# Kernel tuning notes

Measured on AMD Instinct MI355X. Metric: run time of the kernel, lower is better.

## Reference

```python
import jax, jax.numpy as jnp
import numpy as np
import math

B, D_MODEL, SEQ_LEN, EMB_DIM, ORDER = 4, 1024, 4096, 5, 64


def setup_inputs() -> dict:
    key = jax.random.key(0)
    ks = jax.random.split(key, 12)
    L = SEQ_LEN
    # PositionalEmbedding: z = [t, Re(e^{-i f w}), Im(e^{-i f w})]
    t = jnp.linspace(0.0, 1.0, L)[None, :, None]                      # [1,L,1]
    bands = (EMB_DIM - 1) // 2
    t_rescaled = jnp.linspace(0.0, L - 1, L)[None, :, None]           # [1,L,1]
    w = 2 * math.pi * t_rescaled / L
    f = jnp.linspace(1e-4, bands - 1, bands)[None, None]              # [1,1,bands]
    zc = jnp.exp(-1j * f * w.astype(jnp.complex64))                   # [1,L,bands]
    z = jnp.concatenate([t, zc.real, zc.imag], axis=-1)               # [1,L,EMB_DIM]
    # ExponentialModulation deltas (fast_decay_pct=0.3, slow_decay_pct=1.5, target=0.01)
    max_decay = math.log(0.01) / 0.3
    min_decay = math.log(0.01) / 1.5
    deltas = jnp.linspace(min_decay, max_decay, D_MODEL)[None, None]  # [1,1,D]
    s = 0.1  # small init scale for MLP weights
    return {
        "x": jax.random.normal(ks[0], (B, D_MODEL, SEQ_LEN), jnp.float32),
        "L": SEQ_LEN,
        "z": z.astype(jnp.float32),
        "t": t.astype(jnp.float32),
        "deltas": deltas.astype(jnp.float32),
        "W1": jax.random.normal(ks[1], (ORDER, EMB_DIM), jnp.float32) * s,
        "b1": jax.random.normal(ks[2], (ORDER,), jnp.float32) * s,
        "freq": jnp.ones((1, ORDER), jnp.float32),  # Sin freq, w=1
        "W2": jax.random.normal(ks[3], (ORDER, ORDER), jnp.float32) * s,
        "b2": jax.random.normal(ks[4], (ORDER,), jnp.float32) * s,
        "W3": jax.random.normal(ks[5], (ORDER, ORDER), jnp.float32) * s,
        "b3": jax.random.normal(ks[6], (ORDER,), jnp.float32) * s,
        "W4": jax.random.normal(ks[7], (D_MODEL, ORDER), jnp.float32) * s,
        "bias": jax.random.normal(ks[8], (D_MODEL,), jnp.float32),
    }


def reference(x, L, z, t, deltas, W1, b1, freq, W2, b2, W3, b3, W4, bias):
    # --- implicit filter MLP: z [1,L,E] -> k [1,L,D] ---
    zL, tL = z[:, :L], t[:, :L]
    h = jnp.sin(freq * (jnp.einsum('ble,oe->blo', zL, W1) + b1))
    h = jnp.sin(freq * (jnp.einsum('blo,po->blp', h, W2) + b2))
    h = jnp.sin(freq * (jnp.einsum('blo,po->blp', h, W3) + b3))
    h = jnp.einsum('blo,do->bld', h, W4)                # [1,L,D], no bias
    # --- exponential modulation ---
    decay = jnp.exp(-tL * jnp.abs(deltas))              # [1,L,D]
    h = h * decay
    k = h[0].T                                          # [D, L] per-channel filters
    # --- FFT causal conv: irfft(rfft(u)*rfft(k)/n, norm='forward') == plain circular conv on 2L ---
    n = 2 * L
    u_f = jnp.fft.rfft(x, n=n)                          # [B,D,L+1] complex
    k_f = jnp.fft.rfft(k, n=n)                          # [D,L+1]
    y = jnp.fft.irfft(u_f * k_f, n=n)[..., :L]          # [B,D,L]
    out = y + x * bias[:, None]                         # D.unsqueeze(-1) bias term, gelu=False
    return out.astype(x.dtype)
```

## Files before the change

kernel.cpp:

```cpp
#include <hip/hip_runtime.h>
#include <math.h>


#define PAD(i) ((i) + ((i) >> 3))
#define TWO_PI 6.2831853071795864769f

typedef float2 cplx;

__device__ __forceinline__ cplx cmul(cplx a, cplx b) {
    return make_float2(a.x * b.x - a.y * b.y, a.x * b.y + a.y * b.x);
}

__device__ __forceinline__ void dft8(cplx v[8], float sgn) {
    cplx t;
    t = v[1]; v[1] = v[4]; v[4] = t;
    t = v[3]; v[3] = v[6]; v[6] = t;
#pragma unroll
    for (int i = 0; i < 8; i += 2) {
        cplx a = v[i], b = v[i + 1];
        v[i]     = make_float2(a.x + b.x, a.y + b.y);
        v[i + 1] = make_float2(a.x - b.x, a.y - b.y);
    }
#pragma unroll
    for (int i = 0; i < 8; i += 4) {
        cplx a = v[i], b = v[i + 2];
        v[i]     = make_float2(a.x + b.x, a.y + b.y);
        v[i + 2] = make_float2(a.x - b.x, a.y - b.y);
        cplx c1 = v[i + 1], d = v[i + 3];
        cplx dt = make_float2(-sgn * d.y, sgn * d.x);
        v[i + 1] = make_float2(c1.x + dt.x, c1.y + dt.y);
        v[i + 3] = make_float2(c1.x - dt.x, c1.y - dt.y);
    }
    const float C = 0.70710678118654752440f;
    cplx a, b, bt;
    a = v[0]; b = v[4];
    v[0] = make_float2(a.x + b.x, a.y + b.y);
    v[4] = make_float2(a.x - b.x, a.y - b.y);
    a = v[1]; b = v[5]; bt = cmul(b, make_float2(C, sgn * C));
    v[1] = make_float2(a.x + bt.x, a.y + bt.y);
    v[5] = make_float2(a.x - bt.x, a.y - bt.y);
    a = v[2]; b = v[6]; bt = make_float2(-sgn * b.y, sgn * b.x);
    v[2] = make_float2(a.x + bt.x, a.y + bt.y);
    v[6] = make_float2(a.x - bt.x, a.y - bt.y);
    a = v[3]; b = v[7]; bt = cmul(b, make_float2(-C, sgn * C));
    v[3] = make_float2(a.x + bt.x, a.y + bt.y);
    v[7] = make_float2(a.x - bt.x, a.y - bt.y);
}

template <int NS>
__device__ __forceinline__ void fft_pass_ip(cplx* buf, int j, float sgn) {
    cplx v[8];
#pragma unroll
    for (int r = 0; r < 8; r++) v[r] = buf[PAD(j + (r << 9))];
    if (NS > 1) {
        int jm = j & (NS - 1);
        float ang = sgn * (TWO_PI / (float)(NS * 8)) * (float)jm;
#pragma unroll
        for (int r = 1; r < 8; r++) {
            float s, c;
            __sincosf(ang * (float)r, &s, &c);
            v[r] = cmul(v[r], make_float2(c, s));
        }
    }
    dft8(v, sgn);
    __syncthreads();
    int jm2 = j & (NS - 1);
    int base = ((j & ~(NS - 1)) << 3) + jm2;
#pragma unroll
    for (int r = 0; r < 8; r++) buf[PAD(base + r * NS)] = v[r];
    __syncthreads();
}

__device__ __forceinline__ void fft4096_ip(cplx* buf, int t, float sgn) {
    fft_pass_ip<1>(buf, t, sgn);
    fft_pass_ip<8>(buf, t, sgn);
    fft_pass_ip<64>(buf, t, sgn);
    fft_pass_ip<512>(buf, t, sgn);
}

__global__ __launch_bounds__(256) void mlp_kernel(
    const float* __restrict__ zin, const float* __restrict__ W1,
    const float* __restrict__ b1, const float* __restrict__ freq,
    const float* __restrict__ W2, const float* __restrict__ b2,
    const float* __restrict__ W3, const float* __restrict__ b3,
    float* __restrict__ h3T) {
    __shared__ float hs1[64][64];
    __shared__ float hs2[64][64];
    int tid = threadIdx.x;
    int l = tid & 63, w = tid >> 6;
    int lg = blockIdx.x * 64 + l;

    float zf[5];
#pragma unroll
    for (int e = 0; e < 5; e++) zf[e] = zin[lg * 5 + e];

#pragma unroll
    for (int i = 0; i < 16; i++) {
        int o = w * 16 + i;
        float a = b1[o];
#pragma unroll
        for (int e = 0; e < 5; e++) a += W1[o * 5 + e] * zf[e];
        hs1[o][l] = __sinf(freq[o] * a);
    }
    __syncthreads();

    float acc[16];
#pragma unroll
    for (int i = 0; i < 16; i++) acc[i] = b2[w * 16 + i];
#pragma unroll 8
    for (int o = 0; o < 64; o++) {
        float hv = hs1[o][l];
#pragma unroll
        for (int i = 0; i < 16; i++) acc[i] += W2[(w * 16 + i) * 64 + o] * hv;
    }
#pragma unroll
    for (int i = 0; i < 16; i++)
        hs2[w * 16 + i][l] = __sinf(freq[w * 16 + i] * acc[i]);
    __syncthreads();

#pragma unroll
    for (int i = 0; i < 16; i++) acc[i] = b3[w * 16 + i];
#pragma unroll 8
    for (int o = 0; o < 64; o++) {
        float hv = hs2[o][l];
#pragma unroll
        for (int i = 0; i < 16; i++) acc[i] += W3[(w * 16 + i) * 64 + o] * hv;
    }
#pragma unroll
    for (int i = 0; i < 16; i++)
        h3T[(size_t)(w * 16 + i) * 4096 + lg] = __sinf(freq[w * 16 + i] * acc[i]);
}

__global__ __launch_bounds__(256) void kgemm_kernel(
    const float* __restrict__ h3T, const float* __restrict__ W4,
    const float* __restrict__ tvec, const float* __restrict__ deltas,
    float* __restrict__ kout) {
    int lt = blockIdx.x & 15;
    int dt = blockIdx.x >> 4;
    int l = lt * 256 + threadIdx.x;
    float hreg[64];
#pragma unroll
    for (int o = 0; o < 64; o++) hreg[o] = h3T[(size_t)o * 4096 + l];
    float tl = tvec[l];
    const float* W4b = W4 + (size_t)dt * 64 * 64;
    const float* db  = deltas + dt * 64;
#pragma unroll 8
    for (int d = 0; d < 64; d++) {
        float acc = 0.f;
#pragma unroll
        for (int o = 0; o < 64; o++) acc += W4b[d * 64 + o] * hreg[o];
        float dec = __expf(-tl * fabsf(db[d]));
        kout[(size_t)(dt * 64 + d) * 4096 + l] = acc * dec;
    }
}

__global__ __launch_bounds__(512) void filter_fft_kernel(
    const float* __restrict__ kin, float2* __restrict__ Kf) {
    __shared__ cplx buf[4608];
    int d = blockIdx.x, t = threadIdx.x;

    const float4* k4 = (const float4*)(kin + (size_t)d * 4096);
    {
        float4 f0 = k4[2 * t], f1 = k4[2 * t + 1];
        buf[PAD(4 * t + 0)] = make_float2(f0.x, f0.y);
        buf[PAD(4 * t + 1)] = make_float2(f0.z, f0.w);
        buf[PAD(4 * t + 2)] = make_float2(f1.x, f1.y);
        buf[PAD(4 * t + 3)] = make_float2(f1.z, f1.w);
#pragma unroll
        for (int q = 0; q < 4; q++)
            buf[PAD(2048 + 4 * t + q)] = make_float2(0.f, 0.f);
    }
    __syncthreads();
    fft4096_ip(buf, t, -1.0f);

    const float scale = 1.0f / 4096.0f;
    float2* KfRow = Kf + (size_t)d * 4104;
#pragma unroll
    for (int i = 0; i < 4; i++) {
        int k = t + (i << 9);
        if (k == 0) {
            cplx z0 = buf[PAD(0)];
            KfRow[0]    = make_float2((z0.x + z0.y) * scale, 0.f);
            KfRow[4096] = make_float2((z0.x - z0.y) * scale, 0.f);
            cplx zm = buf[PAD(2048)];
            KfRow[2048] = make_float2(zm.x * scale, -zm.y * scale);
        } else {
            int k2 = 4096 - k;
            cplx Zk = buf[PAD(k)], Zq = buf[PAD(k2)];
            cplx Fe = make_float2(0.5f * (Zk.x + Zq.x), 0.5f * (Zk.y - Zq.y));
            cplx Fo = make_float2(0.5f * (Zk.y + Zq.y), -0.5f * (Zk.x - Zq.x));
            float s, c;
            __sincosf(-TWO_PI * (float)k * (1.0f / 8192.0f), &s, &c);
            cplx WFo = cmul(make_float2(c, s), Fo);
            KfRow[k]  = make_float2((Fe.x + WFo.x) * scale, (Fe.y + WFo.y) * scale);
            KfRow[k2] = make_float2((Fe.x - WFo.x) * scale, -(Fe.y - WFo.y) * scale);
        }
    }
}

__global__ __launch_bounds__(512) void conv_kernel(
    const float* __restrict__ x, const float2* __restrict__ Kf,
    const float* __restrict__ bias, float* __restrict__ out) {
    __shared__ cplx buf[4608];
    int rid = blockIdx.x;
    int d = rid & 1023;
    int t = threadIdx.x;
    const float4* x4 = (const float4*)(x + (size_t)rid * 4096);

#pragma unroll
    for (int i = 0; i < 2; i++) {
        int q = t + (i << 9);
        float4 v = x4[q];
        buf[PAD(2 * q)]     = make_float2(v.x, v.y);
        buf[PAD(2 * q + 1)] = make_float2(v.z, v.w);
    }
#pragma unroll
    for (int i = 2; i < 4; i++) {
        int q = t + (i << 9);
        buf[PAD(2 * q)]     = make_float2(0.f, 0.f);
        buf[PAD(2 * q + 1)] = make_float2(0.f, 0.f);
    }
    __syncthreads();
    fft4096_ip(buf, t, -1.0f);

    const float2* KfRow = Kf + (size_t)d * 4104;
#pragma unroll
    for (int i = 0; i < 4; i++) {
        int k = t + (i << 9);
        if (k == 0) {
            cplx z0 = buf[PAD(0)];
            float U0 = z0.x + z0.y;
            float UN = z0.x - z0.y;
            float Y0 = U0 * KfRow[0].x;
            float YN = UN * KfRow[4096].x;
            buf[PAD(0)] = make_float2(0.5f * (Y0 + YN), 0.5f * (Y0 - YN));
            cplx zm = buf[PAD(2048)];
            cplx Um = make_float2(zm.x, -zm.y);
            cplx Ym = cmul(Um, KfRow[2048]);
            buf[PAD(2048)] = make_float2(Ym.x, -Ym.y);
        } else {
            int k2 = 4096 - k;
            cplx Zk = buf[PAD(k)], Zq = buf[PAD(k2)];
            cplx K1 = KfRow[k], K2 = KfRow[k2];
            cplx Fe = make_float2(0.5f * (Zk.x + Zq.x), 0.5f * (Zk.y - Zq.y));
            cplx Fo = make_float2(0.5f * (Zk.y + Zq.y), -0.5f * (Zk.x - Zq.x));
            float s, c;
            __sincosf(-TWO_PI * (float)k * (1.0f / 8192.0f), &s, &c);
            cplx WFo = cmul(make_float2(c, s), Fo);
            cplx U1 = make_float2(Fe.x + WFo.x, Fe.y + WFo.y);
            cplx U2 = make_float2(Fe.x - WFo.x, -(Fe.y - WFo.y));
            cplx Y1 = cmul(U1, K1);
            cplx Y2 = cmul(U2, K2);
            cplx FeY = make_float2(0.5f * (Y1.x + Y2.x), 0.5f * (Y1.y - Y2.y));
            cplx T   = make_float2(0.5f * (Y1.x - Y2.x), 0.5f * (Y1.y + Y2.y));
            cplx FoY = cmul(make_float2(c, -s), T);
            buf[PAD(k)]  = make_float2(FeY.x - FoY.y, FeY.y + FoY.x);
            buf[PAD(k2)] = make_float2(FeY.x + FoY.y, FoY.x - FeY.y);
        }
    }
    __syncthreads();
    fft4096_ip(buf, t, 1.0f);

    float bd = bias[d];
    float4* o4 = (float4*)(out + (size_t)rid * 4096);
#pragma unroll
    for (int i = 0; i < 2; i++) {
        int q = t + (i << 9);
        float4 xv = x4[q];
        cplx za = buf[PAD(2 * q)], zb = buf[PAD(2 * q + 1)];
        float4 o;
        o.x = za.x + xv.x * bd;
        o.y = za.y + xv.y * bd;
        o.z = zb.x + xv.z * bd;
        o.w = zb.y + xv.w * bd;
        o4[q] = o;
    }
}

extern "C" void kernel_launch(void* const* d_in, const int* in_sizes, int n_in,
                              void* d_out, int out_size, void* d_ws, size_t ws_size,
                              hipStream_t stream) {
    const float* x      = (const float*)d_in[0];
    const float* zin    = (const float*)d_in[2];
    const float* tvec   = (const float*)d_in[3];
    const float* deltas = (const float*)d_in[4];
    const float* W1     = (const float*)d_in[5];
    const float* b1     = (const float*)d_in[6];
    const float* freq   = (const float*)d_in[7];
    const float* W2     = (const float*)d_in[8];
    const float* b2     = (const float*)d_in[9];
    const float* W3     = (const float*)d_in[10];
    const float* b3     = (const float*)d_in[11];
    const float* W4     = (const float*)d_in[12];
    const float* bias   = (const float*)d_in[13];
    float* out = (float*)d_out;

    float*  h3T = (float*)d_ws;
    float2* Kf  = (float2*)((char*)d_ws + (size_t)64 * 4096 * sizeof(float));
    float* kbuf = out + (size_t)3072 * 4096;

    mlp_kernel<<<64, 256, 0, stream>>>(zin, W1, b1, freq, W2, b2, W3, b3, h3T);
    kgemm_kernel<<<256, 256, 0, stream>>>(h3T, W4, tvec, deltas, kbuf);
    filter_fft_kernel<<<1024, 512, 0, stream>>>(kbuf, Kf);
    conv_kernel<<<4096, 512, 0, stream>>>(x, Kf, bias, out);
}
```

Before: 272.4 us.

## Fuse first and last FFT passes with global load/store and retile filter GEMM

The first radix-8 FFT pass now loads input directly into registers, exploiting the zero-padded half, so the initial shared-memory staging and one barrier are skipped. The final inverse pass is done in registers and writes the output with the bias term directly, reusing the x values already held in registers instead of rereading x. Only the needed first half of the output is computed and stored. The kgemm kernel is retiled so each thread computes 16 channels by 4 positions with float4 loads and stores, which cuts redundant h3T loads in exchange for more accumulator registers.

```diff
diff --git a/kernel.cpp b/kernel.cpp
--- a/kernel.cpp
+++ b/kernel.cpp
@@ -71,11 +71,16 @@
     __syncthreads();
 }
 
-__device__ __forceinline__ void fft4096_ip(cplx* buf, int t, float sgn) {
-    fft_pass_ip<1>(buf, t, sgn);
-    fft_pass_ip<8>(buf, t, sgn);
-    fft_pass_ip<64>(buf, t, sgn);
-    fft_pass_ip<512>(buf, t, sgn);
+__device__ __forceinline__ void fft_pass1_fwd_regs(cplx* buf, int j, const cplx xv[4]) {
+    cplx v[8];
+#pragma unroll
+    for (int r = 0; r < 4; r++) v[r] = xv[r];
+#pragma unroll
+    for (int r = 4; r < 8; r++) v[r] = make_float2(0.f, 0.f);
+    dft8(v, -1.0f);
+#pragma unroll
+    for (int r = 0; r < 8; r++) buf[PAD(8 * j + r)] = v[r];
+    __syncthreads();
 }
 
 __global__ __launch_bounds__(256) void mlp_kernel(
@@ -135,22 +140,33 @@
     const float* __restrict__ h3T, const float* __restrict__ W4,
     const float* __restrict__ tvec, const float* __restrict__ deltas,
     float* __restrict__ kout) {
-    int lt = blockIdx.x & 15;
-    int dt = blockIdx.x >> 4;
-    int l = lt * 256 + threadIdx.x;
-    float hreg[64];
-#pragma unroll
-    for (int o = 0; o < 64; o++) hreg[o] = h3T[(size_t)o * 4096 + l];
-    float tl = tvec[l];
-    const float* W4b = W4 + (size_t)dt * 64 * 64;
-    const float* db  = deltas + dt * 64;
+    int lt = blockIdx.x & 3;
+    int dt = blockIdx.x >> 2;
+    int l0 = lt * 1024 + threadIdx.x * 4;
+    float4 acc[16];
+#pragma unroll
+    for (int i = 0; i < 16; i++) acc[i] = make_float4(0.f, 0.f, 0.f, 0.f);
 #pragma unroll 8
-    for (int d = 0; d < 64; d++) {
-        float acc = 0.f;
-#pragma unroll
-        for (int o = 0; o < 64; o++) acc += W4b[d * 64 + o] * hreg[o];
-        float dec = __expf(-tl * fabsf(db[d]));
-        kout[(size_t)(dt * 64 + d) * 4096 + l] = acc * dec;
+    for (int o = 0; o < 64; o++) {
+        float4 h = *(const float4*)(h3T + (size_t)o * 4096 + l0);
+#pragma unroll
+        for (int i = 0; i < 16; i++) {
+            float wv = W4[(size_t)(dt * 16 + i) * 64 + o];
+            acc[i].x += wv * h.x; acc[i].y += wv * h.y;
+            acc[i].z += wv * h.z; acc[i].w += wv * h.w;
+        }
+    }
+    float4 tl = *(const float4*)(tvec + l0);
+#pragma unroll
+    for (int i = 0; i < 16; i++) {
+        int d = dt * 16 + i;
+        float da = fabsf(deltas[d]);
+        float4 o;
+        o.x = acc[i].x * __expf(-tl.x * da);
+        o.y = acc[i].y * __expf(-tl.y * da);
+        o.z = acc[i].z * __expf(-tl.z * da);
+        o.w = acc[i].w * __expf(-tl.w * da);
+        *(float4*)(kout + (size_t)d * 4096 + l0) = o;
     }
 }
 
@@ -159,19 +175,14 @@
     __shared__ cplx buf[4608];
     int d = blockIdx.x, t = threadIdx.x;
 
-    const float4* k4 = (const float4*)(kin + (size_t)d * 4096);
-    {
-        float4 f0 = k4[2 * t], f1 = k4[2 * t + 1];
-        buf[PAD(4 * t + 0)] = make_float2(f0.x, f0.y);
-        buf[PAD(4 * t + 1)] = make_float2(f0.z, f0.w);
-        buf[PAD(4 * t + 2)] = make_float2(f1.x, f1.y);
-        buf[PAD(4 * t + 3)] = make_float2(f1.z, f1.w);
-#pragma unroll
-        for (int q = 0; q < 4; q++)
-            buf[PAD(2048 + 4 * t + q)] = make_float2(0.f, 0.f);
-    }
-    __syncthreads();
-    fft4096_ip(buf, t, -1.0f);
+    const cplx* k2 = (const cplx*)(kin + (size_t)d * 4096);
+    cplx xv[4];
+#pragma unroll
+    for (int r = 0; r < 4; r++) xv[r] = k2[t + (r << 9)];
+    fft_pass1_fwd_regs(buf, t, xv);
+    fft_pass_ip<8>(buf, t, -1.0f);
+    fft_pass_ip<64>(buf, t, -1.0f);
+    fft_pass_ip<512>(buf, t, -1.0f);
 
     const float scale = 1.0f / 4096.0f;
     float2* KfRow = Kf + (size_t)d * 4104;
@@ -185,15 +196,15 @@
             cplx zm = buf[PAD(2048)];
             KfRow[2048] = make_float2(zm.x * scale, -zm.y * scale);
         } else {
-            int k2 = 4096 - k;
-            cplx Zk = buf[PAD(k)], Zq = buf[PAD(k2)];
+            int k2i = 4096 - k;
+            cplx Zk = buf[PAD(k)], Zq = buf[PAD(k2i)];
             cplx Fe = make_float2(0.5f * (Zk.x + Zq.x), 0.5f * (Zk.y - Zq.y));
             cplx Fo = make_float2(0.5f * (Zk.y + Zq.y), -0.5f * (Zk.x - Zq.x));
             float s, c;
             __sincosf(-TWO_PI * (float)k * (1.0f / 8192.0f), &s, &c);
             cplx WFo = cmul(make_float2(c, s), Fo);
-            KfRow[k]  = make_float2((Fe.x + WFo.x) * scale, (Fe.y + WFo.y) * scale);
-            KfRow[k2] = make_float2((Fe.x - WFo.x) * scale, -(Fe.y - WFo.y) * scale);
+            KfRow[k]   = make_float2((Fe.x + WFo.x) * scale, (Fe.y + WFo.y) * scale);
+            KfRow[k2i] = make_float2((Fe.x - WFo.x) * scale, -(Fe.y - WFo.y) * scale);
         }
     }
 }
@@ -205,23 +216,15 @@
     int rid = blockIdx.x;
     int d = rid & 1023;
     int t = threadIdx.x;
-    const float4* x4 = (const float4*)(x + (size_t)rid * 4096);
-
-#pragma unroll
-    for (int i = 0; i < 2; i++) {
-        int q = t + (i << 9);
-        float4 v = x4[q];
-        buf[PAD(2 * q)]     = make_float2(v.x, v.y);
-        buf[PAD(2 * q + 1)] = make_float2(v.z, v.w);
-    }
-#pragma unroll
-    for (int i = 2; i < 4; i++) {
-        int q = t + (i << 9);
-        buf[PAD(2 * q)]     = make_float2(0.f, 0.f);
-        buf[PAD(2 * q + 1)] = make_float2(0.f, 0.f);
-    }
-    __syncthreads();
-    fft4096_ip(buf, t, -1.0f);
+
+    const cplx* x2 = (const cplx*)(x + (size_t)rid * 4096);
+    cplx xv[4];
+#pragma unroll
+    for (int r = 0; r < 4; r++) xv[r] = x2[t + (r << 9)];
+    fft_pass1_fwd_regs(buf, t, xv);
+    fft_pass_ip<8>(buf, t, -1.0f);
+    fft_pass_ip<64>(buf, t, -1.0f);
+    fft_pass_ip<512>(buf, t, -1.0f);
 
     const float2* KfRow = Kf + (size_t)d * 4104;
 #pragma unroll
@@ -239,9 +242,9 @@
             cplx Ym = cmul(Um, KfRow[2048]);
             buf[PAD(2048)] = make_float2(Ym.x, -Ym.y);
         } else {
-            int k2 = 4096 - k;
-            cplx Zk = buf[PAD(k)], Zq = buf[PAD(k2)];
-            cplx K1 = KfRow[k], K2 = KfRow[k2];
+            int k2i = 4096 - k;
+            cplx Zk = buf[PAD(k)], Zq = buf[PAD(k2i)];
+            cplx K1 = KfRow[k], K2 = KfRow[k2i];
             cplx Fe = make_float2(0.5f * (Zk.x + Zq.x), 0.5f * (Zk.y - Zq.y));
             cplx Fo = make_float2(0.5f * (Zk.y + Zq.y), -0.5f * (Zk.x - Zq.x));
             float s, c;
@@ -254,26 +257,37 @@
             cplx FeY = make_float2(0.5f * (Y1.x + Y2.x), 0.5f * (Y1.y - Y2.y));
             cplx T   = make_float2(0.5f * (Y1.x - Y2.x), 0.5f * (Y1.y + Y2.y));
             cplx FoY = cmul(make_float2(c, -s), T);
-            buf[PAD(k)]  = make_float2(FeY.x - FoY.y, FeY.y + FoY.x);
-            buf[PAD(k2)] = make_float2(FeY.x + FoY.y, FoY.x - FeY.y);
-        }
-    }
-    __syncthreads();
-    fft4096_ip(buf, t, 1.0f);
-
-    float bd = bias[d];
-    float4* o4 = (float4*)(out + (size_t)rid * 4096);
-#pragma unroll
-    for (int i = 0; i < 2; i++) {
-        int q = t + (i << 9);
-        float4 xv = x4[q];
-        cplx za = buf[PAD(2 * q)], zb = buf[PAD(2 * q + 1)];
-        float4 o;
-        o.x = za.x + xv.x * bd;
-        o.y = za.y + xv.y * bd;
-        o.z = zb.x + xv.z * bd;
-        o.w = zb.y + xv.w * bd;
-        o4[q] = o;
+            buf[PAD(k)]   = make_float2(FeY.x - FoY.y, FeY.y + FoY.x);
+            buf[PAD(k2i)] = make_float2(FeY.x + FoY.y, FoY.x - FeY.y);
+        }
+    }
+    __syncthreads();
+
+    fft_pass_ip<1>(buf, t, 1.0f);
+    fft_pass_ip<8>(buf, t, 1.0f);
+    fft_pass_ip<64>(buf, t, 1.0f);
+    {
+        cplx v[8];
+#pragma unroll
+        for (int r = 0; r < 8; r++) v[r] = buf[PAD(t + (r << 9))];
+        float ang = (TWO_PI / 4096.0f) * (float)t;
+#pragma unroll
+        for (int r = 1; r < 8; r++) {
+            float s, c;
+            __sincosf(ang * (float)r, &s, &c);
+            v[r] = cmul(v[r], make_float2(c, s));
+        }
+        dft8(v, 1.0f);
+        float bd = bias[d];
+        cplx* o2 = (cplx*)(out + (size_t)rid * 4096);
+#pragma unroll
+        for (int r = 0; r < 4; r++) {
+            int m = t + (r << 9);
+            cplx o;
+            o.x = v[r].x + xv[r].x * bd;
+            o.y = v[r].y + xv[r].y * bd;
+            o2[m] = o;
+        }
     }
 }
 
```

After: 245.0 us. -10.1%, faster.
